# Kernel tuning notes

Hardware: AMD Instinct MI355X
Metric: run time of the kernel (lower is better)

The kernel has to match this reference:

```python
import jax, jax.numpy as jnp
import numpy as np

DIM = 96
HEADS = 4
WS = (2, 7, 7)      # window size (wd, wh, ww)
SS = (1, 3, 3)      # shift size
RES = (16, 56, 56)  # (D, H, W)
BATCH = 4
HIDDEN = 384        # mlp_ratio * dim
EPS = 1e-5


def _rel_pos_index(ws):
    wd, wh, ww = ws
    c = np.stack(np.meshgrid(np.arange(wd), np.arange(wh), np.arange(ww), indexing='ij')).reshape(3, -1)
    r = (c[:, :, None] - c[:, None, :]).transpose(1, 2, 0)  # (N, N, 3)
    r[..., 0] += wd - 1
    r[..., 1] += wh - 1
    r[..., 2] += ww - 1
    r[..., 0] *= (2 * wh - 1) * (2 * ww - 1)
    r[..., 1] *= (2 * ww - 1)
    return r.sum(-1)  # (N, N) int


def _attn_mask(res, ws, ss):
    D, H, W = res
    wd, wh, ww = ws
    sd, sh, sw = ss
    img = np.zeros((D, H, W), np.float32)
    cnt = 0
    for dsl in (slice(0, -wd), slice(-wd, -sd), slice(-sd, None)):
        for hsl in (slice(0, -wh), slice(-wh, -sh), slice(-sh, None)):
            for wsl in (slice(0, -ww), slice(-ww, -sw), slice(-sw, None)):
                img[dsl, hsl, wsl] = cnt
                cnt += 1
    N = wd * wh * ww
    m = img.reshape(D // wd, wd, H // wh, wh, W // ww, ww).transpose(0, 2, 4, 1, 3, 5).reshape(-1, N)
    am = m[:, None, :] - m[:, :, None]
    return np.where(am != 0, np.float32(-100.0), np.float32(0.0))  # (nW, N, N)


def setup_inputs() -> dict:
    key = jax.random.key(0)
    ks = jax.random.split(key, 8)
    s = 0.02
    return {
        'x': jax.random.normal(ks[0], (BATCH, DIM) + RES, jnp.float32),
        'gamma1': jnp.ones((DIM,), jnp.float32),
        'beta1': jnp.zeros((DIM,), jnp.float32),
        'gamma2': jnp.ones((DIM,), jnp.float32),
        'beta2': jnp.zeros((DIM,), jnp.float32),
        'qkv_w': jax.random.normal(ks[1], (DIM, 3 * DIM), jnp.float32) * s,
        'qkv_b': jnp.zeros((3 * DIM,), jnp.float32),
        'proj_w': jax.random.normal(ks[2], (DIM, DIM), jnp.float32) * s,
        'proj_b': jnp.zeros((DIM,), jnp.float32),
        'rpb_table': jax.random.normal(ks[3], ((2 * WS[0] - 1) * (2 * WS[1] - 1) * (2 * WS[2] - 1), HEADS), jnp.float32) * s,
        'fc1_w': jax.random.normal(ks[4], (DIM, HIDDEN), jnp.float32) * s,
        'fc1_b': jnp.zeros((HIDDEN,), jnp.float32),
        'fc2_w': jax.random.normal(ks[5], (HIDDEN, DIM), jnp.float32) * s,
        'fc2_b': jnp.zeros((DIM,), jnp.float32),
    }


def _layernorm(t, g, b):
    mu = t.mean(-1, keepdims=True)
    var = ((t - mu) ** 2).mean(-1, keepdims=True)
    return (t - mu) / jnp.sqrt(var + EPS) * g + b


def reference(x, gamma1, beta1, gamma2, beta2, qkv_w, qkv_b, proj_w, proj_b,
              rpb_table, fc1_w, fc1_b, fc2_w, fc2_b):
    B, C, D, H, W = x.shape
    wd, wh, ww = WS
    sd, sh, sw = SS
    N = wd * wh * ww
    nH = HEADS
    dh = C // nH

    rpi = jnp.asarray(_rel_pos_index(WS))          # (N, N) static
    mask = jnp.asarray(_attn_mask(RES, WS, SS))    # (nW, N, N) static
    nW = mask.shape[0]

    xl = jnp.transpose(x, (0, 2, 3, 4, 1))  # (B, D, H, W, C) channels-last

    # norm1 + cyclic shift
    h = _layernorm(xl, gamma1, beta1)
    h = jnp.roll(h, (-sd, -sh, -sw), axis=(1, 2, 3))

    # window partition -> (B*nW, N, C)
    win = h.reshape(B, D // wd, wd, H // wh, wh, W // ww, ww, C)
    win = win.transpose(0, 1, 3, 5, 2, 4, 6, 7).reshape(-1, N, C)

    # window attention
    qkv = (win @ qkv_w + qkv_b).reshape(-1, N, 3, nH, dh).transpose(2, 0, 3, 1, 4)
    q, k, v = qkv[0] * (dh ** -0.5), qkv[1], qkv[2]  # (B_, nH, N, dh)
    attn = jnp.einsum('bhnd,bhmd->bhnm', q, k)       # (B_, nH, N, N)
    rpb = rpb_table[rpi].transpose(2, 0, 1)          # (nH, N, N)
    attn = attn + rpb[None]
    attn = attn.reshape(B, nW, nH, N, N) + mask[None, :, None]
    attn = jax.nn.softmax(attn.reshape(-1, nH, N, N), axis=-1)
    out = jnp.einsum('bhnm,bhmd->bhnd', attn, v).transpose(0, 2, 1, 3).reshape(-1, N, C)
    out = out @ proj_w + proj_b

    # window reverse + reverse shift
    out = out.reshape(B, D // wd, H // wh, W // ww, wd, wh, ww, C)
    out = out.transpose(0, 1, 4, 2, 5, 3, 6, 7).reshape(B, D, H, W, C)
    out = jnp.roll(out, (sd, sh, sw), axis=(1, 2, 3))

    xl = xl + out  # residual 1

    # norm2 + 1x1-conv FFN (pointwise = matmul over channel)
    h2 = _layernorm(xl, gamma2, beta2)
    h2 = jax.nn.gelu(h2 @ fc1_w + fc1_b, approximate=False) @ fc2_w + fc2_b
    xl = xl + h2  # residual 2

    return jnp.transpose(xl, (0, 4, 1, 2, 3))  # back to (B, C, D, H, W)
```

## Files before the change

kernel.cpp:

```cpp
#include <hip/hip_runtime.h>
#include <hip/hip_bf16.h>
#include <cmath>

#define C_DIM 96
#define RES_D 16
#define RES_H 56
#define RES_W 56
#define BATCH 4
#define SPATIAL (RES_D*RES_H*RES_W)
#define NTOK (BATCH*SPATIAL)
#define NWIN_TOT 2048
#define EPS_LN 1e-5f
#define QSCALE 0.2041241452319315f

#define MPAD 112

#define OFF_P   0
#define OFF_Q   14336
#define OFF_K   28672
#define OFF_VT  43008
#define SM_TOT  59392

typedef float f32x4 __attribute__((ext_vector_type(4)));
typedef short s16x8 __attribute__((ext_vector_type(8)));
typedef unsigned u32x4 __attribute__((ext_vector_type(4)));
typedef unsigned u32x2 __attribute__((ext_vector_type(2)));
typedef unsigned short u16;

__device__ __forceinline__ u16 f2bf(float f) {
    unsigned u = __float_as_uint(f);
    u = (u + 0x7FFF + ((u >> 16) & 1)) >> 16;
    return (u16)u;
}
__device__ __forceinline__ int swzP(int r, int c) {
    return r * 128 + ((((c >> 3) ^ (r & 15)) << 3) | (c & 7));
}
__device__ __forceinline__ int swzQ(int r, int c) {
    return r * 32 + ((((c >> 3) ^ ((r >> 1) & 3)) << 3) | (c & 7));
}

__device__ __forceinline__ float wave_reduce_sum(float v) {
#pragma unroll
    for (int off = 32; off > 0; off >>= 1) v += __shfl_xor(v, off, 64);
    return v;
}

__global__ __launch_bounds__(256) void k_prep(
    const float* __restrict__ qkv_w, const float* __restrict__ proj_w,
    const float* __restrict__ fc1_w, const float* __restrict__ fc2_w,
    const float* __restrict__ rpb_table,
    u16* __restrict__ wq, u16* __restrict__ wp, u16* __restrict__ w1,
    u16* __restrict__ w2, float* __restrict__ rpbm) {
    int i = blockIdx.x * 256 + threadIdx.x;
    if (i < 27648) {
        int j = i / 96, c = i % 96;
        wq[i] = f2bf(qkv_w[c * 288 + j]);
    } else if (i < 36864) {
        int t = i - 27648; int j = t / 96, c = t % 96;
        wp[t] = f2bf(proj_w[c * 96 + j]);
    } else if (i < 73728) {
        int t = i - 36864; int j = t / 96, c = t % 96;
        w1[t] = f2bf(fc1_w[c * 384 + j]);
    } else if (i < 110592) {
        int t = i - 73728; int c = t / 384, j = t % 384;
        w2[t] = f2bf(fc2_w[j * 96 + c]);
    } else if (i < 176128) {
        int t = i - 110592;
        int h = t / 16384, r = t % 16384, n = r / 128, m = r % 128;
        float v;
        if (m >= 98) {
            v = -30000.0f;
        } else if (n >= 98) {
            v = 0.0f;
        } else {
            int dzn = n / 49, rn = n % 49, hyn = rn / 7, wxn = rn % 7;
            int dzm = m / 49, rm = m % 49, hym = rm / 7, wxm = rm % 7;
            int ridx = (dzn - dzm + 1) * 169 + (hyn - hym + 6) * 13 + (wxn - wxm + 6);
            v = rpb_table[ridx * 4 + h];
        }
        rpbm[t] = v;
    }
}

__global__ __launch_bounds__(256) void k_transpose_in(const float* __restrict__ x,
                                                      float* __restrict__ xl) {
    __shared__ float tile[32][33];
    const int b = blockIdx.z;
    const int s0 = blockIdx.x * 32;
    const int c0 = blockIdx.y * 32;
    const float* xb = x + (size_t)b * C_DIM * SPATIAL;
    float* xlb = xl + (size_t)b * SPATIAL * C_DIM;
    const int ts = threadIdx.x, tc = threadIdx.y;
#pragma unroll
    for (int i = 0; i < 32; i += 8)
        tile[tc + i][ts] = xb[(size_t)(c0 + tc + i) * SPATIAL + s0 + ts];
    __syncthreads();
#pragma unroll
    for (int i = 0; i < 32; i += 8)
        xlb[(size_t)(s0 + tc + i) * C_DIM + c0 + ts] = tile[ts][tc + i];
}

__global__ __launch_bounds__(448, 2) void k_win_attn(
    const float* __restrict__ xl, float* __restrict__ xl2,
    const float* __restrict__ g1, const float* __restrict__ b1,
    const u16* __restrict__ wqkv, const float* __restrict__ qkv_b,
    const u16* __restrict__ wproj, const float* __restrict__ proj_b,
    const float* __restrict__ rpbm) {
    __shared__ __align__(16) u16 sm[SM_TOT];
    __shared__ int s_gtok[MPAD];
    __shared__ int s_reg[MPAD];

    const int tid = threadIdx.x;
    const int lane = tid & 63;
    const int wv = tid >> 6;
    const int g4 = lane >> 4;
    const int c16 = lane & 15;
    const int mt = wv;

    const int wid = blockIdx.x;
    const int b = wid >> 9;
    const int rem = wid & 511;
    const int wdi = rem >> 6, whi = (rem >> 3) & 7, wwi = rem & 7;

    for (int i = tid; i < 7168; i += 448) {
        int c = 24 + (i & 7);
        int hb = (i >> 3) / 112;
        int r = (i >> 3) % 112;
        int base = (hb < 4) ? (OFF_Q + hb * 3584) : (OFF_K + (hb - 4) * 3584);
        sm[base + swzQ(r, c)] = 0;
    }
    for (int i = tid; i < 4096; i += 448) {
        int h = i >> 10, rr = 24 + ((i >> 7) & 7), c = i & 127;
        sm[OFF_VT + h * 4096 + swzP(rr, c)] = 0;
    }
    for (int i = tid; i < 1536; i += 448) {
        int h = i / 384, r = (i % 384) >> 4, c = 112 + (i & 15);
        sm[OFF_VT + h * 4096 + swzP(r, c)] = 0;
    }
    for (int i = tid; i < 1792; i += 448) {
        int r = i >> 4, c = 112 + (i & 15);
        sm[OFF_P + swzP(r, c)] = 0;
    }
    if (tid < MPAD) {
        if (tid < 98) {
            const int n = tid;
            const int dz = n / 49, r = n % 49, hy = r / 7, wx = r % 7;
            const int rd = wdi * 2 + dz, rh = whi * 7 + hy, rw = wwi * 7 + wx;
            int od = rd + 1; if (od >= RES_D) od -= RES_D;
            int oh = rh + 3; if (oh >= RES_H) oh -= RES_H;
            int ow = rw + 3; if (ow >= RES_W) ow -= RES_W;
            s_gtok[n] = ((b * RES_D + od) * RES_H + oh) * RES_W + ow;
            const int gd = (rd < 14) ? 0 : (rd < 15 ? 1 : 2);
            const int gh = (rh < 49) ? 0 : (rh < 53 ? 1 : 2);
            const int gw = (rw < 49) ? 0 : (rw < 53 ? 1 : 2);
            s_reg[n] = gd * 9 + gh * 3 + gw;
        } else { s_gtok[tid] = 0; s_reg[tid] = -1; }
    }
    __syncthreads();

    const int myrow = mt * 16 + c16;
    const float live = (myrow < 98) ? 1.0f : 0.0f;
    u32x4 xa[3];
    {
        const float* src = xl + (size_t)s_gtok[myrow] * C_DIM;
        f32x4 xv0 = *(const f32x4*)(src + 0 * 32 + g4 * 8);
        f32x4 xv1 = *(const f32x4*)(src + 0 * 32 + g4 * 8 + 4);
        f32x4 xv2 = *(const f32x4*)(src + 1 * 32 + g4 * 8);
        f32x4 xv3 = *(const f32x4*)(src + 1 * 32 + g4 * 8 + 4);
        f32x4 xv4 = *(const f32x4*)(src + 2 * 32 + g4 * 8);
        f32x4 xv5 = *(const f32x4*)(src + 2 * 32 + g4 * 8 + 4);
        float lsum = (xv0[0]+xv0[1]+xv0[2]+xv0[3]) + (xv1[0]+xv1[1]+xv1[2]+xv1[3])
                   + (xv2[0]+xv2[1]+xv2[2]+xv2[3]) + (xv3[0]+xv3[1]+xv3[2]+xv3[3])
                   + (xv4[0]+xv4[1]+xv4[2]+xv4[3]) + (xv5[0]+xv5[1]+xv5[2]+xv5[3]);
        lsum += __shfl_xor(lsum, 16, 64);
        lsum += __shfl_xor(lsum, 32, 64);
        const float mu = lsum * (1.0f / 96.0f);
        f32x4 d0 = xv0 - mu, d1 = xv1 - mu, d2 = xv2 - mu,
              d3 = xv3 - mu, d4 = xv4 - mu, d5 = xv5 - mu;
        float lvv = (d0[0]*d0[0]+d0[1]*d0[1]+d0[2]*d0[2]+d0[3]*d0[3])
                  + (d1[0]*d1[0]+d1[1]*d1[1]+d1[2]*d1[2]+d1[3]*d1[3])
                  + (d2[0]*d2[0]+d2[1]*d2[1]+d2[2]*d2[2]+d2[3]*d2[3])
                  + (d3[0]*d3[0]+d3[1]*d3[1]+d3[2]*d3[2]+d3[3]*d3[3])
                  + (d4[0]*d4[0]+d4[1]*d4[1]+d4[2]*d4[2]+d4[3]*d4[3])
                  + (d5[0]*d5[0]+d5[1]*d5[1]+d5[2]*d5[2]+d5[3]*d5[3]);
        lvv += __shfl_xor(lvv, 16, 64);
        lvv += __shfl_xor(lvv, 32, 64);
        const float rstd = rsqrtf(lvv * (1.0f / 96.0f) + EPS_LN) * live;
#pragma unroll
        for (int ks = 0; ks < 3; ++ks) {
            const f32x4 ea = (ks == 0) ? d0 : (ks == 1) ? d2 : d4;
            const f32x4 eb = (ks == 0) ? d1 : (ks == 1) ? d3 : d5;
            f32x4 ga = *(const f32x4*)(g1 + ks * 32 + g4 * 8);
            f32x4 gb = *(const f32x4*)(g1 + ks * 32 + g4 * 8 + 4);
            f32x4 ba = *(const f32x4*)(b1 + ks * 32 + g4 * 8);
            f32x4 bb = *(const f32x4*)(b1 + ks * 32 + g4 * 8 + 4);
            f32x4 y0 = ea * rstd * ga + ba * live;
            f32x4 y1 = eb * rstd * gb + bb * live;
            xa[ks][0] = (unsigned)f2bf(y0[0]) | ((unsigned)f2bf(y0[1]) << 16);
            xa[ks][1] = (unsigned)f2bf(y0[2]) | ((unsigned)f2bf(y0[3]) << 16);
            xa[ks][2] = (unsigned)f2bf(y1[0]) | ((unsigned)f2bf(y1[1]) << 16);
            xa[ks][3] = (unsigned)f2bf(y1[2]) | ((unsigned)f2bf(y1[3]) << 16);
        }
    }

#pragma unroll
    for (int sel = 0; sel < 3; ++sel) {
#pragma unroll
        for (int t = 0; t < 6; ++t) {
            const int nt = sel * 6 + t;
            f32x4 acc = {0.f, 0.f, 0.f, 0.f};
#pragma unroll
            for (int ks = 0; ks < 3; ++ks) {
                s16x8 a = __builtin_bit_cast(s16x8, xa[ks]);
                s16x8 bw = *(const s16x8*)(wqkv + (size_t)(nt * 16 + c16) * 96 + ks * 32 + g4 * 8);
                acc = __builtin_amdgcn_mfma_f32_16x16x32_bf16(a, bw, acc, 0, 0, 0);
            }
            const float bias = qkv_b[nt * 16 + c16];
            float v0 = acc[0] + bias, v1 = acc[1] + bias, v2 = acc[2] + bias, v3 = acc[3] + bias;
            if (sel == 0) { v0 *= QSCALE; v1 *= QSCALE; v2 *= QSCALE; v3 *= QSCALE; }
            const int j96 = t * 16 + c16;
            const int h = j96 / 24, d = j96 - h * 24;
            const int row0 = mt * 16 + g4 * 4;
            if (sel == 0) {
                sm[OFF_Q + h * 3584 + swzQ(row0 + 0, d)] = f2bf(v0);
                sm[OFF_Q + h * 3584 + swzQ(row0 + 1, d)] = f2bf(v1);
                sm[OFF_Q + h * 3584 + swzQ(row0 + 2, d)] = f2bf(v2);
                sm[OFF_Q + h * 3584 + swzQ(row0 + 3, d)] = f2bf(v3);
            } else if (sel == 1) {
                sm[OFF_K + h * 3584 + swzQ(row0 + 0, d)] = f2bf(v0);
                sm[OFF_K + h * 3584 + swzQ(row0 + 1, d)] = f2bf(v1);
                sm[OFF_K + h * 3584 + swzQ(row0 + 2, d)] = f2bf(v2);
                sm[OFF_K + h * 3584 + swzQ(row0 + 3, d)] = f2bf(v3);
            } else {
                sm[OFF_VT + h * 4096 + swzP(d, row0 + 0)] = f2bf(v0);
                sm[OFF_VT + h * 4096 + swzP(d, row0 + 1)] = f2bf(v1);
                sm[OFF_VT + h * 4096 + swzP(d, row0 + 2)] = f2bf(v2);
                sm[OFF_VT + h * 4096 + swzP(d, row0 + 3)] = f2bf(v3);
            }
        }
    }
    __syncthreads();

    unsigned ogp[4][2][2];
    const int rbase = mt * 16 + g4 * 4;
    int rgs[4];
#pragma unroll
    for (int r = 0; r < 4; ++r) rgs[r] = s_reg[rbase + r];
#pragma unroll
    for (int h = 0; h < 4; ++h) {
        const s16x8 aq = *(const s16x8*)&sm[OFF_Q + h * 3584 + swzQ(mt * 16 + c16, g4 * 8)];
        const float* rh = rpbm + h * 16384;
        float smr[4] = {0.f, 0.f, 0.f, 0.f};
#pragma unroll
        for (int nt = 0; nt < 7; ++nt) {
            s16x8 bk = *(const s16x8*)&sm[OFF_K + h * 3584 + swzQ(nt * 16 + c16, g4 * 8)];
            f32x4 z = {0.f, 0.f, 0.f, 0.f};
            f32x4 sc = __builtin_amdgcn_mfma_f32_16x16x32_bf16(aq, bk, z, 0, 0, 0);
            const int col = nt * 16 + c16;
            const int creg = s_reg[col];
#pragma unroll
            for (int r = 0; r < 4; ++r) {
                float s = sc[r] + rh[(rbase + r) * 128 + col];
                if (rgs[r] != creg) s -= 100.0f;
                const float e = __expf(s);
                sc[r] = e;
                smr[r] += e;
            }
            sm[OFF_P + swzP(rbase + 0, col)] = f2bf(sc[0]);
            sm[OFF_P + swzP(rbase + 1, col)] = f2bf(sc[1]);
            sm[OFF_P + swzP(rbase + 2, col)] = f2bf(sc[2]);
            sm[OFF_P + swzP(rbase + 3, col)] = f2bf(sc[3]);
        }
#pragma unroll
        for (int r = 0; r < 4; ++r) {
#pragma unroll
            for (int m = 1; m <= 8; m <<= 1) smr[r] += __shfl_xor(smr[r], m, 64);
            smr[r] = 1.0f / fmaxf(smr[r], 1e-30f);
        }
#pragma unroll
        for (int dt = 0; dt < 2; ++dt) {
            f32x4 acc = {0.f, 0.f, 0.f, 0.f};
#pragma unroll
            for (int ks = 0; ks < 4; ++ks) {
                s16x8 ap = *(const s16x8*)&sm[OFF_P + swzP(mt * 16 + c16, ks * 32 + g4 * 8)];
                s16x8 bv = *(const s16x8*)&sm[OFF_VT + h * 4096 + swzP(dt * 16 + c16, ks * 32 + g4 * 8)];
                acc = __builtin_amdgcn_mfma_f32_16x16x32_bf16(ap, bv, acc, 0, 0, 0);
            }
            ogp[h][dt][0] = (unsigned)f2bf(acc[0] * smr[0]) | ((unsigned)f2bf(acc[1] * smr[1]) << 16);
            ogp[h][dt][1] = (unsigned)f2bf(acc[2] * smr[2]) | ((unsigned)f2bf(acc[3] * smr[3]) << 16);
        }
    }

#pragma unroll
    for (int h = 0; h < 4; ++h) {
#pragma unroll
        for (int dt = 0; dt < 2; ++dt) {
            const int d = dt * 16 + c16;
            if (d < 24) {
                const int col = h * 24 + d;
#pragma unroll
                for (int rp = 0; rp < 2; ++rp) {
                    const unsigned u = ogp[h][dt][rp];
                    const int row0 = mt * 16 + g4 * 4 + rp * 2;
                    sm[OFF_P + swzP(row0, col)] = (u16)u;
                    sm[OFF_P + swzP(row0 + 1, col)] = (u16)(u >> 16);
                }
            }
        }
    }

#pragma unroll
    for (int nt = 0; nt < 6; ++nt) {
        f32x4 acc = {0.f, 0.f, 0.f, 0.f};
#pragma unroll
        for (int ks = 0; ks < 3; ++ks) {
            s16x8 a = *(const s16x8*)&sm[OFF_P + swzP(mt * 16 + c16, ks * 32 + g4 * 8)];
            s16x8 bw = *(const s16x8*)(wproj + (size_t)(nt * 16 + c16) * 96 + ks * 32 + g4 * 8);
            acc = __builtin_amdgcn_mfma_f32_16x16x32_bf16(a, bw, acc, 0, 0, 0);
        }
        const int col = nt * 16 + c16;
        const float pb = proj_b[col];
#pragma unroll
        for (int r = 0; r < 4; ++r) {
            const int row = mt * 16 + g4 * 4 + r;
            if (row < 98) {
                const size_t base = (size_t)s_gtok[row] * C_DIM + col;
                xl2[base] = xl[base] + acc[r] + pb;
            }
        }
    }
}

__global__ __launch_bounds__(256, 6) void k_ffn(
    const float* __restrict__ xl2, float* __restrict__ out,
    const float* __restrict__ g2, const float* __restrict__ b2,
    const u16* __restrict__ w1, const float* __restrict__ fc1_b,
    const u16* __restrict__ w2, const float* __restrict__ fc2_b) {
    __shared__ __align__(16) u16 sg[32 * 384];
    float* s_res = (float*)sg;

    const int tid = threadIdx.x;
    const int lane = tid & 63;
    const int wave = tid >> 6;
    const int g4 = lane >> 4, c16 = lane & 15;
    const int mt = wave & 1;
    const int nh = wave >> 1;
    const int t0 = blockIdx.x * 32;
    const int tok = mt * 16 + c16;

    u32x4 xa[3];
    {
        const float* src = xl2 + (size_t)(t0 + tok) * C_DIM;
        f32x4 xv0 = *(const f32x4*)(src + 0 * 32 + g4 * 8);
        f32x4 xv1 = *(const f32x4*)(src + 0 * 32 + g4 * 8 + 4);
        f32x4 xv2 = *(const f32x4*)(src + 1 * 32 + g4 * 8);
        f32x4 xv3 = *(const f32x4*)(src + 1 * 32 + g4 * 8 + 4);
        f32x4 xv4 = *(const f32x4*)(src + 2 * 32 + g4 * 8);
        f32x4 xv5 = *(const f32x4*)(src + 2 * 32 + g4 * 8 + 4);
        float lsum = (xv0[0]+xv0[1]+xv0[2]+xv0[3]) + (xv1[0]+xv1[1]+xv1[2]+xv1[3])
                   + (xv2[0]+xv2[1]+xv2[2]+xv2[3]) + (xv3[0]+xv3[1]+xv3[2]+xv3[3])
                   + (xv4[0]+xv4[1]+xv4[2]+xv4[3]) + (xv5[0]+xv5[1]+xv5[2]+xv5[3]);
        lsum += __shfl_xor(lsum, 16, 64);
        lsum += __shfl_xor(lsum, 32, 64);
        const float mu = lsum * (1.0f / 96.0f);
        f32x4 d0 = xv0 - mu, d1 = xv1 - mu, d2 = xv2 - mu,
              d3 = xv3 - mu, d4 = xv4 - mu, d5 = xv5 - mu;
        float lvv = (d0[0]*d0[0]+d0[1]*d0[1]+d0[2]*d0[2]+d0[3]*d0[3])
                  + (d1[0]*d1[0]+d1[1]*d1[1]+d1[2]*d1[2]+d1[3]*d1[3])
                  + (d2[0]*d2[0]+d2[1]*d2[1]+d2[2]*d2[2]+d2[3]*d2[3])
                  + (d3[0]*d3[0]+d3[1]*d3[1]+d3[2]*d3[2]+d3[3]*d3[3])
                  + (d4[0]*d4[0]+d4[1]*d4[1]+d4[2]*d4[2]+d4[3]*d4[3])
                  + (d5[0]*d5[0]+d5[1]*d5[1]+d5[2]*d5[2]+d5[3]*d5[3]);
        lvv += __shfl_xor(lvv, 16, 64);
        lvv += __shfl_xor(lvv, 32, 64);
        const float rstd = rsqrtf(lvv * (1.0f / 96.0f) + EPS_LN);
#pragma unroll
        for (int ks = 0; ks < 3; ++ks) {
            const f32x4 ea = (ks == 0) ? d0 : (ks == 1) ? d2 : d4;
            const f32x4 eb = (ks == 0) ? d1 : (ks == 1) ? d3 : d5;
            f32x4 ga = *(const f32x4*)(g2 + ks * 32 + g4 * 8);
            f32x4 gb = *(const f32x4*)(g2 + ks * 32 + g4 * 8 + 4);
            f32x4 ba = *(const f32x4*)(b2 + ks * 32 + g4 * 8);
            f32x4 bb = *(const f32x4*)(b2 + ks * 32 + g4 * 8 + 4);
            f32x4 y0 = ea * rstd * ga + ba;
            f32x4 y1 = eb * rstd * gb + bb;
            xa[ks][0] = (unsigned)f2bf(y0[0]) | ((unsigned)f2bf(y0[1]) << 16);
            xa[ks][1] = (unsigned)f2bf(y0[2]) | ((unsigned)f2bf(y0[3]) << 16);
            xa[ks][2] = (unsigned)f2bf(y1[0]) | ((unsigned)f2bf(y1[1]) << 16);
            xa[ks][3] = (unsigned)f2bf(y1[2]) | ((unsigned)f2bf(y1[3]) << 16);
        }
    }

#pragma unroll 1
    for (int i = 0; i < 12; ++i) {
        const int nt = nh * 12 + i;
        f32x4 acc = {0.f, 0.f, 0.f, 0.f};
#pragma unroll
        for (int ks = 0; ks < 3; ++ks) {
            s16x8 aw = *(const s16x8*)(w1 + (size_t)(nt * 16 + c16) * 96 + ks * 32 + g4 * 8);
            s16x8 bx = __builtin_bit_cast(s16x8, xa[ks]);
            acc = __builtin_amdgcn_mfma_f32_16x16x32_bf16(aw, bx, acc, 0, 0, 0);
        }
        const f32x4 bias = *(const f32x4*)(fc1_b + nt * 16 + g4 * 4);
        float gv[4];
#pragma unroll
        for (int r = 0; r < 4; ++r) {
            const float v = acc[r] + bias[r];
            gv[r] = 0.5f * v * (1.0f + erff(v * 0.70710678118654752f));
        }
        const unsigned lo = (unsigned)f2bf(gv[0]) | ((unsigned)f2bf(gv[1]) << 16);
        const unsigned hi = (unsigned)f2bf(gv[2]) | ((unsigned)f2bf(gv[3]) << 16);
        const int chunk = (2 * nt + (g4 >> 1)) ^ (tok & 15);
        u32x2 pk = {lo, hi};
        *(u32x2*)&sg[tok * 384 + chunk * 8 + (g4 & 1) * 4] = pk;
    }
    __syncthreads();

    f32x4 facc[3];
#pragma unroll 1
    for (int i = 0; i < 3; ++i) {
        const int nt = nh * 3 + i;
        f32x4 acc = {0.f, 0.f, 0.f, 0.f};
#pragma unroll
        for (int ks = 0; ks < 12; ++ks) {
            s16x8 aw = *(const s16x8*)(w2 + (size_t)(nt * 16 + c16) * 384 + ks * 32 + g4 * 8);
            s16x8 bg = *(const s16x8*)&sg[tok * 384 + (((ks * 4 + g4) ^ (tok & 15)) << 3)];
            acc = __builtin_amdgcn_mfma_f32_16x16x32_bf16(aw, bg, acc, 0, 0, 0);
        }
        const f32x4 bias = *(const f32x4*)(fc2_b + nt * 16 + g4 * 4);
        const f32x4 res = *(const f32x4*)(xl2 + (size_t)(t0 + tok) * C_DIM + nt * 16 + g4 * 4);
        facc[i] = acc + bias + res;
    }
    __syncthreads();
#pragma unroll
    for (int i = 0; i < 3; ++i) {
        const int nt = nh * 3 + i;
        *(f32x4*)&s_res[tok * 100 + nt * 16 + g4 * 4] = facc[i];
    }
    __syncthreads();

    const int bb = t0 / SPATIAL;
    const int sbase = t0 % SPATIAL;
    for (int idx = tid; idx < 96 * 32; idx += 256) {
        const int c = idx >> 5, tk = idx & 31;
        out[((size_t)bb * C_DIM + c) * SPATIAL + sbase + tk] = s_res[tk * 100 + c];
    }
}

extern "C" void kernel_launch(void* const* d_in, const int* in_sizes, int n_in,
                              void* d_out, int out_size, void* d_ws, size_t ws_size,
                              hipStream_t stream) {
    const float* x      = (const float*)d_in[0];
    const float* g1     = (const float*)d_in[1];
    const float* be1    = (const float*)d_in[2];
    const float* g2     = (const float*)d_in[3];
    const float* be2    = (const float*)d_in[4];
    const float* qkv_w  = (const float*)d_in[5];
    const float* qkv_b  = (const float*)d_in[6];
    const float* proj_w = (const float*)d_in[7];
    const float* proj_b = (const float*)d_in[8];
    const float* rpb    = (const float*)d_in[9];
    const float* fc1_w  = (const float*)d_in[10];
    const float* fc1_b  = (const float*)d_in[11];
    const float* fc2_w  = (const float*)d_in[12];
    const float* fc2_b  = (const float*)d_in[13];
    float* out = (float*)d_out;

    float* xl  = (float*)d_ws;
    float* xl2 = xl + (size_t)NTOK * C_DIM;
    u16* wq = (u16*)(xl2 + (size_t)NTOK * C_DIM);
    u16* wp = wq + 27648;
    u16* w1 = wp + 9216;
    u16* w2 = w1 + 36864;
    float* rpbm = (float*)(w2 + 36864);

    k_prep<<<688, 256, 0, stream>>>(qkv_w, proj_w, fc1_w, fc2_w, rpb, wq, wp, w1, w2, rpbm);
    k_transpose_in<<<dim3(SPATIAL / 32, C_DIM / 32, BATCH), dim3(32, 8), 0, stream>>>(x, xl);
    k_win_attn<<<NWIN_TOT, 448, 0, stream>>>(xl, xl2, g1, be1, wq, qkv_b, wp, proj_b, rpbm);
    k_ffn<<<NTOK / 32, 256, 0, stream>>>(xl2, out, g2, be2, w1, fc1_b, w2, fc2_b);
}
```

Measured before the change: 442.9 us.

## Double FFN token tile to 64 per block and vectorize transposed output stores

New measurement: 378.0 us. 1.17x faster.

```diff
diff --git a/kernel.cpp b/kernel.cpp
--- a/kernel.cpp
+++ b/kernel.cpp
@@ -331,25 +331,26 @@
     }
 }
 
-__global__ __launch_bounds__(256, 6) void k_ffn(
+__global__ __launch_bounds__(256, 3) void k_ffn(
     const float* __restrict__ xl2, float* __restrict__ out,
     const float* __restrict__ g2, const float* __restrict__ b2,
     const u16* __restrict__ w1, const float* __restrict__ fc1_b,
     const u16* __restrict__ w2, const float* __restrict__ fc2_b) {
-    __shared__ __align__(16) u16 sg[32 * 384];
+    __shared__ __align__(16) u16 sg[64 * 384];
     float* s_res = (float*)sg;
 
     const int tid = threadIdx.x;
     const int lane = tid & 63;
     const int wave = tid >> 6;
     const int g4 = lane >> 4, c16 = lane & 15;
-    const int mt = wave & 1;
+    const int mg = wave & 1;
     const int nh = wave >> 1;
-    const int t0 = blockIdx.x * 32;
-    const int tok = mt * 16 + c16;
-
-    u32x4 xa[3];
-    {
+    const int t0 = blockIdx.x * 64;
+
+    u32x4 xa[2][3];
+#pragma unroll
+    for (int g = 0; g < 2; ++g) {
+        const int tok = mg * 32 + g * 16 + c16;
         const float* src = xl2 + (size_t)(t0 + tok) * C_DIM;
         f32x4 xv0 = *(const f32x4*)(src + 0 * 32 + g4 * 8);
         f32x4 xv1 = *(const f32x4*)(src + 0 * 32 + g4 * 8 + 4);
@@ -384,66 +385,91 @@
             f32x4 bb = *(const f32x4*)(b2 + ks * 32 + g4 * 8 + 4);
             f32x4 y0 = ea * rstd * ga + ba;
             f32x4 y1 = eb * rstd * gb + bb;
-            xa[ks][0] = (unsigned)f2bf(y0[0]) | ((unsigned)f2bf(y0[1]) << 16);
-            xa[ks][1] = (unsigned)f2bf(y0[2]) | ((unsigned)f2bf(y0[3]) << 16);
-            xa[ks][2] = (unsigned)f2bf(y1[0]) | ((unsigned)f2bf(y1[1]) << 16);
-            xa[ks][3] = (unsigned)f2bf(y1[2]) | ((unsigned)f2bf(y1[3]) << 16);
+            xa[g][ks][0] = (unsigned)f2bf(y0[0]) | ((unsigned)f2bf(y0[1]) << 16);
+            xa[g][ks][1] = (unsigned)f2bf(y0[2]) | ((unsigned)f2bf(y0[3]) << 16);
+            xa[g][ks][2] = (unsigned)f2bf(y1[0]) | ((unsigned)f2bf(y1[1]) << 16);
+            xa[g][ks][3] = (unsigned)f2bf(y1[2]) | ((unsigned)f2bf(y1[3]) << 16);
         }
     }
 
 #pragma unroll 1
     for (int i = 0; i < 12; ++i) {
         const int nt = nh * 12 + i;
-        f32x4 acc = {0.f, 0.f, 0.f, 0.f};
+        f32x4 acc0 = {0.f, 0.f, 0.f, 0.f};
+        f32x4 acc1 = {0.f, 0.f, 0.f, 0.f};
 #pragma unroll
         for (int ks = 0; ks < 3; ++ks) {
             s16x8 aw = *(const s16x8*)(w1 + (size_t)(nt * 16 + c16) * 96 + ks * 32 + g4 * 8);
-            s16x8 bx = __builtin_bit_cast(s16x8, xa[ks]);
-            acc = __builtin_amdgcn_mfma_f32_16x16x32_bf16(aw, bx, acc, 0, 0, 0);
+            acc0 = __builtin_amdgcn_mfma_f32_16x16x32_bf16(aw, __builtin_bit_cast(s16x8, xa[0][ks]), acc0, 0, 0, 0);
+            acc1 = __builtin_amdgcn_mfma_f32_16x16x32_bf16(aw, __builtin_bit_cast(s16x8, xa[1][ks]), acc1, 0, 0, 0);
         }
         const f32x4 bias = *(const f32x4*)(fc1_b + nt * 16 + g4 * 4);
-        float gv[4];
-#pragma unroll
-        for (int r = 0; r < 4; ++r) {
-            const float v = acc[r] + bias[r];
-            gv[r] = 0.5f * v * (1.0f + erff(v * 0.70710678118654752f));
-        }
-        const unsigned lo = (unsigned)f2bf(gv[0]) | ((unsigned)f2bf(gv[1]) << 16);
-        const unsigned hi = (unsigned)f2bf(gv[2]) | ((unsigned)f2bf(gv[3]) << 16);
-        const int chunk = (2 * nt + (g4 >> 1)) ^ (tok & 15);
-        u32x2 pk = {lo, hi};
-        *(u32x2*)&sg[tok * 384 + chunk * 8 + (g4 & 1) * 4] = pk;
+#pragma unroll
+        for (int g = 0; g < 2; ++g) {
+            const f32x4 acc = (g == 0) ? acc0 : acc1;
+            const int tok = mg * 32 + g * 16 + c16;
+            float gv[4];
+#pragma unroll
+            for (int r = 0; r < 4; ++r) {
+                const float v = acc[r] + bias[r];
+                gv[r] = 0.5f * v * (1.0f + erff(v * 0.70710678118654752f));
+            }
+            const unsigned lo = (unsigned)f2bf(gv[0]) | ((unsigned)f2bf(gv[1]) << 16);
+            const unsigned hi = (unsigned)f2bf(gv[2]) | ((unsigned)f2bf(gv[3]) << 16);
+            const int chunk = (2 * nt + (g4 >> 1)) ^ (tok & 15);
+            u32x2 pk = {lo, hi};
+            *(u32x2*)&sg[tok * 384 + chunk * 8 + (g4 & 1) * 4] = pk;
+        }
     }
     __syncthreads();
 
-    f32x4 facc[3];
+    f32x4 facc[3][2];
+    const int tokA = mg * 32 + c16;
+    const int tokB = tokA + 16;
 #pragma unroll 1
     for (int i = 0; i < 3; ++i) {
         const int nt = nh * 3 + i;
-        f32x4 acc = {0.f, 0.f, 0.f, 0.f};
+        f32x4 a0 = {0.f, 0.f, 0.f, 0.f};
+        f32x4 a1 = {0.f, 0.f, 0.f, 0.f};
 #pragma unroll
         for (int ks = 0; ks < 12; ++ks) {
             s16x8 aw = *(const s16x8*)(w2 + (size_t)(nt * 16 + c16) * 384 + ks * 32 + g4 * 8);
-            s16x8 bg = *(const s16x8*)&sg[tok * 384 + (((ks * 4 + g4) ^ (tok & 15)) << 3)];
-            acc = __builtin_amdgcn_mfma_f32_16x16x32_bf16(aw, bg, acc, 0, 0, 0);
+            s16x8 bg0 = *(const s16x8*)&sg[tokA * 384 + (((ks * 4 + g4) ^ (tokA & 15)) << 3)];
+            s16x8 bg1 = *(const s16x8*)&sg[tokB * 384 + (((ks * 4 + g4) ^ (tokB & 15)) << 3)];
+            a0 = __builtin_amdgcn_mfma_f32_16x16x32_bf16(aw, bg0, a0, 0, 0, 0);
+            a1 = __builtin_amdgcn_mfma_f32_16x16x32_bf16(aw, bg1, a1, 0, 0, 0);
         }
         const f32x4 bias = *(const f32x4*)(fc2_b + nt * 16 + g4 * 4);
-        const f32x4 res = *(const f32x4*)(xl2 + (size_t)(t0 + tok) * C_DIM + nt * 16 + g4 * 4);
-        facc[i] = acc + bias + res;
+        const f32x4 resA = *(const f32x4*)(xl2 + (size_t)(t0 + tokA) * C_DIM + nt * 16 + g4 * 4);
+        const f32x4 resB = *(const f32x4*)(xl2 + (size_t)(t0 + tokB) * C_DIM + nt * 16 + g4 * 4);
+        facc[i][0] = a0 + bias + resA;
+        facc[i][1] = a1 + bias + resB;
     }
     __syncthreads();
+
 #pragma unroll
     for (int i = 0; i < 3; ++i) {
         const int nt = nh * 3 + i;
-        *(f32x4*)&s_res[tok * 100 + nt * 16 + g4 * 4] = facc[i];
+#pragma unroll
+        for (int g = 0; g < 2; ++g) {
+            const int tok = mg * 32 + g * 16 + c16;
+#pragma unroll
+            for (int r = 0; r < 4; ++r)
+                s_res[tok * 97 + nt * 16 + g4 * 4 + r] = facc[i][g][r];
+        }
     }
     __syncthreads();
 
     const int bb = t0 / SPATIAL;
     const int sbase = t0 % SPATIAL;
-    for (int idx = tid; idx < 96 * 32; idx += 256) {
-        const int c = idx >> 5, tk = idx & 31;
-        out[((size_t)bb * C_DIM + c) * SPATIAL + sbase + tk] = s_res[tk * 100 + c];
+    for (int e = tid; e < 1536; e += 256) {
+        const int c = e >> 4, tq = e & 15;
+        f32x4 v;
+        v[0] = s_res[(tq * 4 + 0) * 97 + c];
+        v[1] = s_res[(tq * 4 + 1) * 97 + c];
+        v[2] = s_res[(tq * 4 + 2) * 97 + c];
+        v[3] = s_res[(tq * 4 + 3) * 97 + c];
+        *(f32x4*)&out[((size_t)bb * C_DIM + c) * SPATIAL + sbase + tq * 4] = v;
     }
 }
 
@@ -477,5 +503,5 @@
     k_prep<<<688, 256, 0, stream>>>(qkv_w, proj_w, fc1_w, fc2_w, rpb, wq, wp, w1, w2, rpbm);
     k_transpose_in<<<dim3(SPATIAL / 32, C_DIM / 32, BATCH), dim3(32, 8), 0, stream>>>(x, xl);
     k_win_attn<<<NWIN_TOT, 448, 0, stream>>>(xl, xl2, g1, be1, wq, qkv_b, wp, proj_b, rpbm);
-    k_ffn<<<NTOK / 32, 256, 0, stream>>>(xl2, out, g2, be2, w1, fc1_b, w2, fc2_b);
-}
+    k_ffn<<<NTOK / 64, 256, 0, stream>>>(xl2, out, g2, be2, w1, fc1_b, w2, fc2_b);
+}
```
